# Kernel optimization log

Hardware: AMD Instinct MI355X
Metric: run time of the kernel (lower is better)

## Reference

```python
import jax, jax.numpy as jnp
import numpy as np

B, S, T = 1024, 1024, 32
TAGS = ["O"] + [p + f"T{i}" for i in range(1, 16) for p in ("B-", "I-")] + ["B-T16"]
MASKED = -1.0e4


def _init_params(key):
    bound = float(np.sqrt(6.0 / T))
    k1, k2, k3 = jax.random.split(key, 3)
    start = np.array(jax.random.uniform(k1, (T,), minval=-bound, maxval=bound))
    trans = np.array(jax.random.uniform(k2, (T, T), minval=-bound, maxval=bound))
    end = np.array(jax.random.uniform(k3, (T,), minval=-bound, maxval=bound))
    # structural BIO masking, as in _initialize_parameters
    for i, src in enumerate(TAGS):
        if src.startswith("I-"):
            start[i] = MASKED
        for j, tgt in enumerate(TAGS):
            if (src.startswith("B-") or src.startswith("I-")) and tgt.startswith("I-") and src[2:] != tgt[2:]:
                trans[i, j] = MASKED
            elif src == "O" and tgt.startswith("I-"):
                trans[i, j] = MASKED
    return jnp.asarray(start, jnp.float32), jnp.asarray(trans, jnp.float32), jnp.asarray(end, jnp.float32)


def setup_inputs() -> dict:
    key = jax.random.key(0)
    k_em, k_tag, k_len, k_par = jax.random.split(key, 4)
    emissions = jax.random.normal(k_em, (B, S, T), dtype=jnp.float32)
    tags = jax.random.randint(k_tag, (B, S), 0, T, dtype=jnp.int64) if jax.config.jax_enable_x64 else jax.random.randint(k_tag, (B, S), 0, T).astype(jnp.int32)
    lengths = jax.random.randint(k_len, (B,), S // 4, S + 1)
    mask = jnp.arange(S)[None, :] < lengths[:, None]  # prefix mask, bool [B, S]
    start_transitions, transitions, end_transitions = _init_params(k_par)
    return {
        "emissions": emissions,
        "tags": tags,
        "mask": mask,
        "start_transitions": start_transitions,
        "transitions": transitions,
        "end_transitions": end_transitions,
    }


def reference(emissions, tags, mask, start_transitions, transitions, end_transitions):
    b, s, t = emissions.shape
    ar = jnp.arange(s)
    bidx = jnp.arange(b)
    head = jnp.min(jnp.where(mask, ar[None, :], s - 1), axis=1)  # [B]
    tail = jnp.max(ar[None, :] * mask, axis=1)                   # [B]
    nonempty = mask.sum(axis=1) != 0

    # condition[:, j-1] == (mask[:, j] and head != j), for j = 1..S-1
    cond = mask[:, 1:] & (head[:, None] != ar[None, 1:])  # [B, S-1]

    # ---- numerator (gold path score): additive, fully vectorized ----
    head_tags = tags[bidx, head]
    tail_tags = tags[bidx, tail]
    em_tag = jnp.take_along_axis(emissions, tags[:, :, None], axis=2)[:, :, 0]  # [B, S]
    trans_step = transitions[tags[:, :-1], tags[:, 1:]]                          # [B, S-1]
    numerator = (start_transitions[head_tags]
                 + em_tag[bidx, head]
                 + jnp.sum(jnp.where(cond, trans_step + em_tag[:, 1:], 0.0), axis=1)
                 + end_transitions[tail_tags])
    numerator = jnp.where(nonempty, numerator, 0.0)

    # ---- denominator (log partition): scan over time ----
    score0 = start_transitions[None, :] + emissions[bidx, head]  # [B, T]

    def step(score, xs):
        em_j, cond_j = xs  # [B, T], [B]
        nxt = jax.nn.logsumexp(score[:, :, None] + transitions[None, :, :] + em_j[:, None, :], axis=1)
        return jnp.where(cond_j[:, None], nxt, score), None

    em_seq = jnp.moveaxis(emissions[:, 1:, :], 1, 0)  # [S-1, B, T]
    cond_seq = jnp.moveaxis(cond, 1, 0)               # [S-1, B]
    score_final, _ = jax.lax.scan(step, score0, (em_seq, cond_seq))
    denominator = jax.nn.logsumexp(score_final + end_transitions[None, :], axis=1)
    denominator = jnp.where(nonempty, denominator, 0.0)

    # ---- token_mean reduction ----
    llh = denominator - numerator
    labels = mask.sum(axis=1).astype(emissions.dtype)
    eps = 1e-6
    return jnp.sum(llh / (labels + eps)) / (jnp.sum(labels != 0).astype(emissions.dtype) + eps)
```

## Files before the change

kernel.cpp:

```cpp
#include <hip/hip_runtime.h>
#include <cstdint>

static constexpr int S = 1024;
static constexpr int T = 32;
static constexpr float L2E  = 1.4426950408889634f;
static constexpr float LN2f = 0.6931471805599453f;

typedef __attribute__((ext_vector_type(8)))  short  short8;
typedef __attribute__((ext_vector_type(16))) float  float16;

union Frag { unsigned u[4]; short8 s; };

__global__ void crf_zero(float* ws) {
  ws[0] = 0.0f; ws[1] = 0.0f; ((unsigned*)ws)[2] = 0u;
}

__device__ __forceinline__ float bcast_lane(float v, int k) {
  return __uint_as_float((unsigned)__builtin_amdgcn_readlane((int)__float_as_uint(v), k));
}

__device__ __forceinline__ unsigned pk2(float lo, float hi) {
#if __has_builtin(__builtin_amdgcn_cvt_pk_bf16_f32)
  typedef __attribute__((ext_vector_type(2))) __bf16 bf162_t;
  union { bf162_t v; unsigned u; } r;
  r.v = __builtin_amdgcn_cvt_pk_bf16_f32(lo, hi);
  return r.u;
#else
  unsigned h_ = __float_as_uint(hi), l_ = __float_as_uint(lo);
  return ((h_ + 0x8000u) & 0xFFFF0000u) | ((l_ + 0x8000u) >> 16);
#endif
}

__device__ __forceinline__ void plswap(unsigned& x, unsigned& y, bool hih) {
#if __has_builtin(__builtin_amdgcn_permlane32_swap)
  auto r = __builtin_amdgcn_permlane32_swap((int)x, (int)y, false, false);
  x = (unsigned)r[0]; y = (unsigned)r[1];
#else
  unsigned ex = (unsigned)__shfl_xor((int)x, 32, 64);
  unsigned ey = (unsigned)__shfl_xor((int)y, 32, 64);
  unsigned nx = hih ? ey : x;
  unsigned ny = hih ? y  : ex;
  x = nx; y = ny;
#endif
}

__global__ __launch_bounds__(512, 4) void crf_main(
    const float* __restrict__ em, const int* __restrict__ tags,
    const int* __restrict__ mask, const float* __restrict__ startT,
    const float* __restrict__ trans, const float* __restrict__ endT,
    float* __restrict__ ws, float* __restrict__ out, int B)
{
  __shared__ __align__(16) float    s_g[8 * 512];
  __shared__ __align__(16) unsigned s_mats[8 * 544];
  __shared__ float s_trans[1024];
  __shared__ short s_tags[1024];
  __shared__ unsigned long long s_mb[17];
  __shared__ int   s_head, s_tail, s_cnt, s_K[8];
  __shared__ float s_num[8];

  const int tid = threadIdx.x;
  const int l   = tid & 63;
  const int wv  = tid >> 6;
  const int b   = blockIdx.x;
  const int n   = l & 31;
  const int h   = l >> 5;
  const bool hih = (h == 1);

  const float* emb   = em   + (size_t)b * S * T;
  const int*   maskb = mask + (size_t)b * S;
  const int*   tagsb = tags + (size_t)b * S;

  for (int i = tid; i < 1024; i += 512) {
    s_tags[i]  = (short)tagsb[i];
    s_trans[i] = trans[i];
  }
  {
    unsigned long long b0 = __ballot(maskb[wv * 128 + l] != 0);
    unsigned long long b1 = __ballot(maskb[wv * 128 + 64 + l] != 0);
    if (l == 0) { s_mb[2 * wv] = b0; s_mb[2 * wv + 1] = b1; }
    if (tid == 0) s_mb[16] = 0ull;
  }

  Frag Alo, Ahi;
  #pragma unroll
  for (int p = 0; p < 4; ++p) {
    int k0 = 8 * h + 2 * p;
    Alo.u[p] = pk2(exp2f(trans[(k0 + 0)  * T + n] * L2E),
                   exp2f(trans[(k0 + 1)  * T + n] * L2E));
    Ahi.u[p] = pk2(exp2f(trans[(k0 + 16) * T + n] * L2E),
                   exp2f(trans[(k0 + 17) * T + n] * L2E));
  }
  __syncthreads();

  if (wv == 0) {
    int first = 0x7fffffff, last = -1, pc = 0;
    if (l < 16) {
      unsigned long long w = s_mb[l];
      if (w) {
        first = 64 * l + (int)__builtin_ctzll(w);
        last  = 64 * l + 63 - (int)__builtin_clzll(w);
        pc    = (int)__builtin_popcountll(w);
      }
    }
    #pragma unroll
    for (int d = 1; d < 64; d <<= 1) {
      first = min(first, __shfl_xor(first, d));
      last  = max(last,  __shfl_xor(last,  d));
      pc   += __shfl_xor(pc, d);
    }
    if (l == 0) { s_head = first; s_tail = last; s_cnt = pc; }
  }
  __syncthreads();
  const int cnt  = s_cnt;
  const int head = (cnt > 0) ? s_head : 0;
  const int tail = (cnt > 0) ? s_tail : 0;

  const int span = tail - head;
  const int Lc   = (span + 7) >> 3;
  const int c0   = head + 1 + wv * Lc;
  const int c1   = min(c0 + Lc, tail + 1);

  float* sgw = s_g + wv * 512;
  Frag Blo, Bhi;
  #pragma unroll
  for (int p = 0; p < 4; ++p) {
    int k0 = 8 * h + 2 * p;
    Blo.u[p] = ((k0 == n)      ? 0x3F80u : 0u) | ((k0 + 1  == n) ? 0x3F800000u : 0u);
    Bhi.u[p] = ((k0 + 16 == n) ? 0x3F80u : 0u) | ((k0 + 17 == n) ? 0x3F800000u : 0u);
  }
  int   Kacc  = 0;
  float numer = 0.0f;

#define FOLD(JJ, RSC) do {                                                   \
    const float* gr = sgw + (JJ) * T + 4 * h;                                \
    float4 ga = *(const float4*)(gr);                                        \
    float4 gb = *(const float4*)(gr + 8);                                    \
    float4 gc = *(const float4*)(gr + 16);                                   \
    float4 gd = *(const float4*)(gr + 24);                                   \
    float16 D = {0,0,0,0,0,0,0,0,0,0,0,0,0,0,0,0};                           \
    D = __builtin_amdgcn_mfma_f32_32x32x16_bf16(Alo.s, Blo.s, D, 0, 0, 0);   \
    D = __builtin_amdgcn_mfma_f32_32x32x16_bf16(Ahi.s, Bhi.s, D, 0, 0, 0);   \
    D[0]  *= ga.x; D[1]  *= ga.y; D[2]  *= ga.z; D[3]  *= ga.w;              \
    D[4]  *= gb.x; D[5]  *= gb.y; D[6]  *= gb.z; D[7]  *= gb.w;              \
    D[8]  *= gc.x; D[9]  *= gc.y; D[10] *= gc.z; D[11] *= gc.w;              \
    D[12] *= gd.x; D[13] *= gd.y; D[14] *= gd.z; D[15] *= gd.w;              \
    if (RSC) {                                                               \
      float mx = fmaxf(fmaxf(fmaxf(D[0], D[1]), fmaxf(D[2], D[3])),          \
                       fmaxf(fmaxf(D[4], D[5]), fmaxf(D[6], D[7])));         \
      mx = fmaxf(mx, fmaxf(fmaxf(fmaxf(D[8], D[9]),  fmaxf(D[10], D[11])),   \
                           fmaxf(fmaxf(D[12], D[13]), fmaxf(D[14], D[15]))));\
      mx = fmaxf(mx, __shfl_xor(mx, 1));  mx = fmaxf(mx, __shfl_xor(mx, 2)); \
      mx = fmaxf(mx, __shfl_xor(mx, 4));  mx = fmaxf(mx, __shfl_xor(mx, 8)); \
      mx = fmaxf(mx, __shfl_xor(mx, 16)); mx = fmaxf(mx, __shfl_xor(mx, 32));\
      int E = (int)((__float_as_uint(mx) >> 23) & 0xffu);                    \
      float sc = __uint_as_float((unsigned)(254 - E) << 23);                 \
      Kacc += E - 127;                                                       \
      _Pragma("unroll")                                                      \
      for (int q_ = 0; q_ < 16; ++q_) D[q_] *= sc;                           \
    }                                                                        \
    unsigned u0 = pk2(D[0],  D[1]),  u1 = pk2(D[2],  D[3]);                  \
    unsigned u2 = pk2(D[4],  D[5]),  u3 = pk2(D[6],  D[7]);                  \
    unsigned u4 = pk2(D[8],  D[9]),  u5 = pk2(D[10], D[11]);                 \
    unsigned u6 = pk2(D[12], D[13]), u7 = pk2(D[14], D[15]);                 \
    plswap(u0, u2, hih); plswap(u1, u3, hih);                                \
    plswap(u4, u6, hih); plswap(u5, u7, hih);                                \
    Blo.u[0] = u0; Blo.u[1] = u1; Blo.u[2] = u2; Blo.u[3] = u3;              \
    Bhi.u[0] = u4; Bhi.u[1] = u5; Bhi.u[2] = u6; Bhi.u[3] = u7;              \
  } while (0)

  for (int j0 = c0; j0 < c1; j0 += 16) {
    const int ns = min(16, c1 - j0);
    const int w = j0 >> 6, o = j0 & 63;
    unsigned long long bits = s_mb[w] >> o;
    if (o) bits |= s_mb[w + 1] << (64 - o);
    unsigned eff = (unsigned)(bits & 0xFFFFull) & (unsigned)((1u << ns) - 1u);

    {
      const int i0 = l, i1 = l + 64;
      const int r0 = min(j0 + (i0 >> 3), S - 1), q0 = i0 & 7;
      const int r1 = min(j0 + (i1 >> 3), S - 1), q1 = i1 & 7;
      float4 v0 = ((const float4*)(emb + (size_t)r0 * T))[q0];
      float4 v1 = ((const float4*)(emb + (size_t)r1 * T))[q1];
      v0.x = exp2f(v0.x * L2E); v0.y = exp2f(v0.y * L2E);
      v0.z = exp2f(v0.z * L2E); v0.w = exp2f(v0.w * L2E);
      v1.x = exp2f(v1.x * L2E); v1.y = exp2f(v1.y * L2E);
      v1.z = exp2f(v1.z * L2E); v1.w = exp2f(v1.w * L2E);
      ((float4*)sgw)[i0] = v0; ((float4*)sgw)[i1] = v1;
    }

    if (l < ns && ((eff >> l) & 1u)) {
      int j  = j0 + l;
      int tg = (int)s_tags[j], tp = (int)s_tags[j - 1];
      numer += s_trans[tp * T + tg] + log2f(sgw[l * T + tg]) * LN2f;
    }

    if (eff == 0xFFFFu) {
      #pragma unroll
      for (int jj = 0; jj < 16; ++jj) FOLD(jj, ((jj & 7) == 7));
    } else {
      for (int jj = 0; jj < ns; ++jj)
        if ((eff >> jj) & 1u) FOLD(jj, true);
    }
  }
#undef FOLD

  {
    unsigned* mw = s_mats + wv * 544;
    #pragma unroll
    for (int p = 0; p < 4; ++p) {
      mw[(4 * h + p)     * 34 + n] = Blo.u[p];
      mw[(4 * h + p + 8) * 34 + n] = Bhi.u[p];
    }
  }
  #pragma unroll
  for (int d = 1; d < 64; d <<= 1) numer += __shfl_xor(numer, d);
  if (l == 0) { s_num[wv] = numer; s_K[wv] = Kacc; }
  __syncthreads();

  if (wv == 0) {
    const int t = n;
    const float em0 = emb[head * T + t];
    float sc0 = (startT[t] + em0) * L2E;
    float m0 = sc0;
    #pragma unroll
    for (int d = 1; d < 32; d <<= 1) m0 = fmaxf(m0, __shfl_xor(m0, d));
    float e = exp2f(sc0 - m0);
    float Mtot = m0;

    const unsigned sh = (t & 1) ? 0u : 16u;
    for (int c = 0; c < 8; ++c) {
      const unsigned* mw = s_mats + c * 544 + (t >> 1) * 34;
      float acc = 0.0f;
      #pragma unroll
      for (int q2 = 0; q2 < 16; ++q2) {
        uint2 w2 = *(const uint2*)(mw + 2 * q2);
        float vlo = __uint_as_float((w2.x << sh) & 0xFFFF0000u);
        float vhi = __uint_as_float((w2.y << sh) & 0xFFFF0000u);
        acc = fmaf(vlo, bcast_lane(e, 2 * q2), acc);
        acc = fmaf(vhi, bcast_lane(e, 2 * q2 + 1), acc);
      }
      e = acc;
      Mtot += (float)s_K[c];
      float mx = e;
      #pragma unroll
      for (int d = 1; d < 32; d <<= 1) mx = fmaxf(mx, __shfl_xor(mx, d));
      int E = (int)((__float_as_uint(mx) >> 23) & 0xffu);
      e *= __uint_as_float((unsigned)(254 - E) << 23);
      Mtot += (float)(E - 127);
    }

    float fv = e * exp2f(endT[t] * L2E);
    #pragma unroll
    for (int d = 1; d < 32; d <<= 1) fv += __shfl_xor(fv, d);
    float denom = (Mtot + log2f(fv)) * LN2f;

    if (l == 0) {
      if (cnt > 0) {
        float ntot = 0.0f;
        for (int wq = 0; wq < 8; ++wq) ntot += s_num[wq];
        int th = (int)s_tags[head], tt = (int)s_tags[tail];
        ntot += startT[th] + bcast_lane(em0, th) + endT[tt];
        atomicAdd(&ws[0], (denom - ntot) / ((float)cnt + 1e-6f));
        atomicAdd(&ws[1], 1.0f);
      }
      __threadfence();
      unsigned done = atomicAdd((unsigned*)ws + 2, 1u);
      if (done == (unsigned)(B - 1)) {
        __threadfence();
        out[0] = ws[0] / (ws[1] + 1e-6f);
      }
    }
  }
}

extern "C" void kernel_launch(void* const* d_in, const int* in_sizes, int n_in,
                              void* d_out, int out_size, void* d_ws, size_t ws_size,
                              hipStream_t stream) {
  const float* em     = (const float*)d_in[0];
  const int*   tags   = (const int*)d_in[1];
  const int*   mask   = (const int*)d_in[2];
  const float* startT = (const float*)d_in[3];
  const float* trans  = (const float*)d_in[4];
  const float* endT   = (const float*)d_in[5];
  float* out = (float*)d_out;
  float* ws  = (float*)d_ws;

  const int B = in_sizes[0] / (S * T);

  crf_zero<<<1, 1, 0, stream>>>(ws);
  crf_main<<<B, 512, 0, stream>>>(em, tags, mask, startT, trans, endT, ws, out, B);
}
```

Before: 303.6 us.

## Permute state index order to drop permlane swaps and store exp-emissions as bf16

Reorders the tag index space through a permutation (sig) applied to the transition matrix, the identity seed and the final matrix store. The MFMA output layout then feeds directly into the next B operand, which removes the permlane32 swaps from every serial fold step. The exponentiated emission tile in shared memory is also stored as packed bf16 instead of fp32, halving LDS traffic and footprint. This costs extra precision loss on the emission factors, including the numerator log term, which now reads a bf16-rounded value.

Result: faster. 283.3 us (-6.7%).

```diff
diff --git a/kernel.cpp b/kernel.cpp
--- a/kernel.cpp
+++ b/kernel.cpp
@@ -19,7 +19,7 @@
   return __uint_as_float((unsigned)__builtin_amdgcn_readlane((int)__float_as_uint(v), k));
 }
 
-__device__ __forceinline__ unsigned pk2(float lo, float hi) {
+__device__ __forceinline__ unsigned pk2r(float lo, float hi) {
 #if __has_builtin(__builtin_amdgcn_cvt_pk_bf16_f32)
   typedef __attribute__((ext_vector_type(2))) __bf16 bf162_t;
   union { bf162_t v; unsigned u; } r;
@@ -31,17 +31,21 @@
 #endif
 }
 
-__device__ __forceinline__ void plswap(unsigned& x, unsigned& y, bool hih) {
-#if __has_builtin(__builtin_amdgcn_permlane32_swap)
-  auto r = __builtin_amdgcn_permlane32_swap((int)x, (int)y, false, false);
-  x = (unsigned)r[0]; y = (unsigned)r[1];
+__device__ __forceinline__ unsigned pk2f(float lo, float hi) {
+#if __has_builtin(__builtin_amdgcn_cvt_pk_bf16_f32)
+  return pk2r(lo, hi);
 #else
-  unsigned ex = (unsigned)__shfl_xor((int)x, 32, 64);
-  unsigned ey = (unsigned)__shfl_xor((int)y, 32, 64);
-  unsigned nx = hih ? ey : x;
-  unsigned ny = hih ? y  : ex;
-  x = nx; y = ny;
+  return __builtin_amdgcn_perm(__float_as_uint(hi), __float_as_uint(lo), 0x07060302u);
 #endif
+}
+
+__device__ __forceinline__ float lo16(unsigned w) { return __uint_as_float(w << 16); }
+__device__ __forceinline__ float hi16(unsigned w) { return __uint_as_float(w & 0xFFFF0000u); }
+
+__device__ __forceinline__ int sig(int k) {
+  int g2 = (k >> 2) & 3;
+  if (g2 == 1) g2 = 2; else if (g2 == 2) g2 = 1;
+  return (k & ~12) | (g2 << 2);
 }
 
 __global__ __launch_bounds__(512, 4) void crf_main(
@@ -50,7 +54,7 @@
     const float* __restrict__ trans, const float* __restrict__ endT,
     float* __restrict__ ws, float* __restrict__ out, int B)
 {
-  __shared__ __align__(16) float    s_g[8 * 512];
+  __shared__ __align__(16) unsigned s_g16[8 * 256];
   __shared__ __align__(16) unsigned s_mats[8 * 544];
   __shared__ float s_trans[1024];
   __shared__ short s_tags[1024];
@@ -64,7 +68,6 @@
   const int b   = blockIdx.x;
   const int n   = l & 31;
   const int h   = l >> 5;
-  const bool hih = (h == 1);
 
   const float* emb   = em   + (size_t)b * S * T;
   const int*   maskb = mask + (size_t)b * S;
@@ -85,10 +88,10 @@
   #pragma unroll
   for (int p = 0; p < 4; ++p) {
     int k0 = 8 * h + 2 * p;
-    Alo.u[p] = pk2(exp2f(trans[(k0 + 0)  * T + n] * L2E),
-                   exp2f(trans[(k0 + 1)  * T + n] * L2E));
-    Ahi.u[p] = pk2(exp2f(trans[(k0 + 16) * T + n] * L2E),
-                   exp2f(trans[(k0 + 17) * T + n] * L2E));
+    Alo.u[p] = pk2r(exp2f(trans[sig(k0 + 0)      * T + n] * L2E),
+                    exp2f(trans[sig(k0 + 1)      * T + n] * L2E));
+    Ahi.u[p] = pk2r(exp2f(trans[sig(16 + k0 + 0) * T + n] * L2E),
+                    exp2f(trans[sig(16 + k0 + 1) * T + n] * L2E));
   }
   __syncthreads();
 
@@ -120,30 +123,33 @@
   const int c0   = head + 1 + wv * Lc;
   const int c1   = min(c0 + Lc, tail + 1);
 
-  float* sgw = s_g + wv * 512;
+  unsigned* sgw16 = s_g16 + wv * 256;
   Frag Blo, Bhi;
   #pragma unroll
   for (int p = 0; p < 4; ++p) {
     int k0 = 8 * h + 2 * p;
-    Blo.u[p] = ((k0 == n)      ? 0x3F80u : 0u) | ((k0 + 1  == n) ? 0x3F800000u : 0u);
-    Bhi.u[p] = ((k0 + 16 == n) ? 0x3F80u : 0u) | ((k0 + 17 == n) ? 0x3F800000u : 0u);
+    Blo.u[p] = ((sig(k0) == n)          ? 0x3F80u : 0u) |
+               ((sig(k0 + 1) == n)      ? 0x3F800000u : 0u);
+    Bhi.u[p] = ((sig(16 + k0) == n)     ? 0x3F80u : 0u) |
+               ((sig(16 + k0 + 1) == n) ? 0x3F800000u : 0u);
   }
   int   Kacc  = 0;
   float numer = 0.0f;
 
 #define FOLD(JJ, RSC) do {                                                   \
-    const float* gr = sgw + (JJ) * T + 4 * h;                                \
-    float4 ga = *(const float4*)(gr);                                        \
-    float4 gb = *(const float4*)(gr + 8);                                    \
-    float4 gc = *(const float4*)(gr + 16);                                   \
-    float4 gd = *(const float4*)(gr + 24);                                   \
+    const uint2* gw = (const uint2*)(sgw16 + (JJ) * 16);                     \
+    uint2 wa = gw[h], wb = gw[h + 2], wc = gw[h + 4], wd = gw[h + 6];        \
     float16 D = {0,0,0,0,0,0,0,0,0,0,0,0,0,0,0,0};                           \
     D = __builtin_amdgcn_mfma_f32_32x32x16_bf16(Alo.s, Blo.s, D, 0, 0, 0);   \
     D = __builtin_amdgcn_mfma_f32_32x32x16_bf16(Ahi.s, Bhi.s, D, 0, 0, 0);   \
-    D[0]  *= ga.x; D[1]  *= ga.y; D[2]  *= ga.z; D[3]  *= ga.w;              \
-    D[4]  *= gb.x; D[5]  *= gb.y; D[6]  *= gb.z; D[7]  *= gb.w;              \
-    D[8]  *= gc.x; D[9]  *= gc.y; D[10] *= gc.z; D[11] *= gc.w;              \
-    D[12] *= gd.x; D[13] *= gd.y; D[14] *= gd.z; D[15] *= gd.w;              \
+    D[0]  *= lo16(wa.x); D[1]  *= hi16(wa.x);                                \
+    D[2]  *= lo16(wa.y); D[3]  *= hi16(wa.y);                                \
+    D[4]  *= lo16(wb.x); D[5]  *= hi16(wb.x);                                \
+    D[6]  *= lo16(wb.y); D[7]  *= hi16(wb.y);                                \
+    D[8]  *= lo16(wc.x); D[9]  *= hi16(wc.x);                                \
+    D[10] *= lo16(wc.y); D[11] *= hi16(wc.y);                                \
+    D[12] *= lo16(wd.x); D[13] *= hi16(wd.x);                                \
+    D[14] *= lo16(wd.y); D[15] *= hi16(wd.y);                                \
     if (RSC) {                                                               \
       float mx = fmaxf(fmaxf(fmaxf(D[0], D[1]), fmaxf(D[2], D[3])),          \
                        fmaxf(fmaxf(D[4], D[5]), fmaxf(D[6], D[7])));         \
@@ -158,14 +164,10 @@
       _Pragma("unroll")                                                      \
       for (int q_ = 0; q_ < 16; ++q_) D[q_] *= sc;                           \
     }                                                                        \
-    unsigned u0 = pk2(D[0],  D[1]),  u1 = pk2(D[2],  D[3]);                  \
-    unsigned u2 = pk2(D[4],  D[5]),  u3 = pk2(D[6],  D[7]);                  \
-    unsigned u4 = pk2(D[8],  D[9]),  u5 = pk2(D[10], D[11]);                 \
-    unsigned u6 = pk2(D[12], D[13]), u7 = pk2(D[14], D[15]);                 \
-    plswap(u0, u2, hih); plswap(u1, u3, hih);                                \
-    plswap(u4, u6, hih); plswap(u5, u7, hih);                                \
-    Blo.u[0] = u0; Blo.u[1] = u1; Blo.u[2] = u2; Blo.u[3] = u3;              \
-    Bhi.u[0] = u4; Bhi.u[1] = u5; Bhi.u[2] = u6; Bhi.u[3] = u7;              \
+    Blo.u[0] = pk2f(D[0],  D[1]);  Blo.u[1] = pk2f(D[2],  D[3]);             \
+    Blo.u[2] = pk2f(D[4],  D[5]);  Blo.u[3] = pk2f(D[6],  D[7]);             \
+    Bhi.u[0] = pk2f(D[8],  D[9]);  Bhi.u[1] = pk2f(D[10], D[11]);            \
+    Bhi.u[2] = pk2f(D[12], D[13]); Bhi.u[3] = pk2f(D[14], D[15]);            \
   } while (0)
 
   for (int j0 = c0; j0 < c1; j0 += 16) {
@@ -181,17 +183,19 @@
       const int r1 = min(j0 + (i1 >> 3), S - 1), q1 = i1 & 7;
       float4 v0 = ((const float4*)(emb + (size_t)r0 * T))[q0];
       float4 v1 = ((const float4*)(emb + (size_t)r1 * T))[q1];
-      v0.x = exp2f(v0.x * L2E); v0.y = exp2f(v0.y * L2E);
-      v0.z = exp2f(v0.z * L2E); v0.w = exp2f(v0.w * L2E);
-      v1.x = exp2f(v1.x * L2E); v1.y = exp2f(v1.y * L2E);
-      v1.z = exp2f(v1.z * L2E); v1.w = exp2f(v1.w * L2E);
-      ((float4*)sgw)[i0] = v0; ((float4*)sgw)[i1] = v1;
+      uint2 p0 = make_uint2(pk2r(exp2f(v0.x * L2E), exp2f(v0.y * L2E)),
+                            pk2r(exp2f(v0.z * L2E), exp2f(v0.w * L2E)));
+      uint2 p1 = make_uint2(pk2r(exp2f(v1.x * L2E), exp2f(v1.y * L2E)),
+                            pk2r(exp2f(v1.z * L2E), exp2f(v1.w * L2E)));
+      ((uint2*)sgw16)[i0] = p0; ((uint2*)sgw16)[i1] = p1;
     }
 
     if (l < ns && ((eff >> l) & 1u)) {
       int j  = j0 + l;
       int tg = (int)s_tags[j], tp = (int)s_tags[j - 1];
-      numer += s_trans[tp * T + tg] + log2f(sgw[l * T + tg]) * LN2f;
+      unsigned gword = sgw16[l * 16 + (tg >> 1)];
+      float gval = (tg & 1) ? hi16(gword) : lo16(gword);
+      numer += s_trans[tp * T + tg] + log2f(gval) * LN2f;
     }
 
     if (eff == 0xFFFFu) {
@@ -208,8 +212,8 @@
     unsigned* mw = s_mats + wv * 544;
     #pragma unroll
     for (int p = 0; p < 4; ++p) {
-      mw[(4 * h + p)     * 34 + n] = Blo.u[p];
-      mw[(4 * h + p + 8) * 34 + n] = Bhi.u[p];
+      mw[(sig(8 * h + 2 * p)      >> 1) * 34 + n] = Blo.u[p];
+      mw[(sig(16 + 8 * h + 2 * p) >> 1) * 34 + n] = Bhi.u[p];
     }
   }
   #pragma unroll
```
